# Optimization experiments

Measured on AMD Instinct MI355X. Metric: run time of the kernel, lower is better.

Reference implementation:

```python
import math
import jax, jax.numpy as jnp
import numpy as np

K = 1.0            # Lorentz manifold curvature k
B, S = 4, 2048     # batch, seq_len
IN, H, OUT = 512, 8, 64   # in_channels, num_heads, out_channels (space dim; head_dim = OUT+1)


def setup_inputs() -> dict:
    key = jax.random.key(0)
    ks = jax.random.split(key, 8)
    std = 1.0 / math.sqrt(IN)
    return {
        "query_input": jax.random.normal(ks[0], (B, S, IN), jnp.float32),
        "source_input": jax.random.normal(ks[1], (B, S, IN), jnp.float32),
        # per-head HypLinear weights stacked on a leading head axis: [H, OUT, IN]
        "Wq_w": jax.random.normal(ks[2], (H, OUT, IN), jnp.float32) * std,
        "Wq_b": jnp.zeros((H, OUT), jnp.float32),
        "Wk_w": jax.random.normal(ks[3], (H, OUT, IN), jnp.float32) * std,
        "Wk_b": jnp.zeros((H, OUT), jnp.float32),
        "Wv_w": jax.random.normal(ks[4], (H, OUT, IN), jnp.float32) * std,
        "Wv_b": jnp.zeros((H, OUT), jnp.float32),
        "scale": jnp.array([math.sqrt(OUT)], jnp.float32),  # nn.Parameter([sqrt(out_channels)])
        "bias": jnp.zeros((), jnp.float32),                 # nn.Parameter(zeros(()))
    }


def hyp_linear(x, w, b):
    # HypLinear: linear map to space part, recompute Lorentz time coord sqrt(||x_s||^2 + k)
    sp = jnp.einsum('bsi,hoi->bsho', x, w) + b            # [B,S,H,OUT]
    t = jnp.sqrt(jnp.sum(sp * sp, axis=-1, keepdims=True) + K)
    return jnp.concatenate([t, sp], axis=-1)              # [B,S,H,OUT+1]


def reference(query_input, source_input, Wq_w, Wq_b, Wk_w, Wk_b, Wv_w, Wv_b, scale, bias):
    q = hyp_linear(query_input, Wq_w, Wq_b)   # [B,S,H,D], D = OUT+1
    k = hyp_linear(source_input, Wk_w, Wk_b)
    v = hyp_linear(source_input, Wv_w, Wv_b)

    # Lorentzian cinner: <x,y>_L = -x0*y0 + <x_s, y_s>
    sgn = jnp.concatenate([-jnp.ones((1,), q.dtype), jnp.ones((OUT,), q.dtype)])
    att = jnp.einsum('bqhd,bkhd->bhqk', q * sgn, k)       # [B,H,S,S]
    att = (2.0 + 2.0 * att) / scale[0] + bias

    causal = jnp.triu(jnp.full((S, S), -1e9, q.dtype), 1)  # causal mask (additive)
    att = jax.nn.softmax(att + causal, axis=-1)

    ctx = jnp.einsum('bhqk,bkhd->bqhd', att, v)           # [B,S,H,D]

    # manifold.mid_point over the heads axis (dim=-2)
    ave = jnp.mean(ctx, axis=2)                           # [B,S,D]
    inner = -ave[..., :1] ** 2 + jnp.sum(ave[..., 1:] ** 2, axis=-1, keepdims=True)
    denom = jnp.sqrt(jnp.maximum(jnp.abs(-inner), 1e-8))
    return math.sqrt(K) * ave / denom                     # [B,S,D]
```

## Files before the change

### kernel.cpp

```cpp
#include <hip/hip_runtime.h>

#define BATCH 4
#define SEQ   2048
#define INC   512
#define NH    8
#define OUTC  64
#define DD    65
#define NROW  (BATCH * NH * SEQ)

typedef float f32x4 __attribute__((ext_vector_type(4)));
typedef short short8 __attribute__((ext_vector_type(8)));
typedef short short4v __attribute__((ext_vector_type(4)));
typedef unsigned short us;

static __device__ __forceinline__ us f2b(float f) {
  unsigned int u = __float_as_uint(f);
  u = (u + 0x7FFFu + ((u >> 16) & 1u)) >> 16;
  return (us)u;
}
static __device__ __forceinline__ float b2f(us h) {
  return __uint_as_float(((unsigned int)h) << 16);
}
static __device__ __forceinline__ unsigned int pk2(float lo, float hi) {
  unsigned int r;
  asm("v_cvt_pk_bf16_f32 %0, %1, %2" : "=v"(r) : "v"(lo), "v"(hi));
  return r;
}
static __device__ __forceinline__ short8 mk8(unsigned int a, unsigned int b,
                                             unsigned int c, unsigned int d) {
  union { unsigned int u[4]; short8 s; } x;
  x.u[0] = a; x.u[1] = b; x.u[2] = c; x.u[3] = d;
  return x.s;
}

#define GLDS(g, l) __builtin_amdgcn_global_load_lds( \
    (const __attribute__((address_space(1))) void*)(g), \
    (__attribute__((address_space(3))) void*)(l), 16, 0, 0)
#define SB() __builtin_amdgcn_sched_barrier(0)

__global__ __launch_bounds__(256) void tobf16_kernel(
    const float* __restrict__ Xq, const float* __restrict__ Xs,
    const float* __restrict__ Wq, const float* __restrict__ Wk,
    const float* __restrict__ Wv,
    us* __restrict__ dXq, us* __restrict__ dXs,
    us* __restrict__ dWq, us* __restrict__ dWk, us* __restrict__ dWv)
{
  const int which = blockIdx.y;
  const float* src;
  us* dst;
  int n;
  switch (which) {
    case 0: src = Xq; dst = dXq; n = BATCH * SEQ * INC; break;
    case 1: src = Xs; dst = dXs; n = BATCH * SEQ * INC; break;
    case 2: src = Wq; dst = dWq; n = NH * OUTC * INC; break;
    case 3: src = Wk; dst = dWk; n = NH * OUTC * INC; break;
    default: src = Wv; dst = dWv; n = NH * OUTC * INC; break;
  }
  for (long i = (long)blockIdx.x * 256 + threadIdx.x; i * 4 < n;
       i += (long)gridDim.x * 256) {
    f32x4 v = *(const f32x4*)(src + i * 4);
    short4v o;
    o[0] = (short)f2b(v[0]); o[1] = (short)f2b(v[1]);
    o[2] = (short)f2b(v[2]); o[3] = (short)f2b(v[3]);
    *(short4v*)(dst + i * 4) = o;
  }
}

__global__ __launch_bounds__(256) void proj_kernel(
    const us* __restrict__ Xqb, const us* __restrict__ Xsb,
    const us* __restrict__ Wqb, const us* __restrict__ Wkb, const us* __restrict__ Wvb,
    const float* __restrict__ Bq, const float* __restrict__ Bk, const float* __restrict__ Bv,
    const float* __restrict__ scale_p,
    us* __restrict__ qs, unsigned int* __restrict__ qta,
    us* __restrict__ ks, unsigned int* __restrict__ kta,
    us* __restrict__ vs, us* __restrict__ vtc)
{
  const int which = blockIdx.z;
  const us* X = (which == 0) ? Xqb : Xsb;
  const us* W = (which == 0) ? Wqb : (which == 1 ? Wkb : Wvb);
  const float* Bb = (which == 0) ? Bq : (which == 1 ? Bk : Bv);
  us* outs = (which == 0) ? qs : (which == 1 ? ks : vs);
  const float al2 = (2.0f / scale_p[0]) * 1.44269504088896f;
  const float oscale = (which == 0) ? al2 : 1.0f;

  const int lin = blockIdx.x;
  const int h   = (lin >> 3) & 7;
  const int m0  = (((lin >> 6) << 3) | (lin & 7)) * 64;
  const int n0  = h * 64;

  __shared__ alignas(16) us lX[2][64 * 64];
  __shared__ alignas(16) us lW[2][64 * 64];

  const int tid  = threadIdx.x;
  const int lane = tid & 63;
  const int wave = tid >> 6;
  const int arow = lane & 15;
  const int agrp = lane >> 4;
  const int rl   = lane >> 3;
  const int chx  = ((lane & 7) ^ rl) * 8;
  const int r0   = wave * 8 + rl;
  const int r1   = r0 + 32;

#define PSTAGE(buf, k0) do { \
    GLDS(X + (size_t)(m0 + r0) * INC + (k0) + chx, &lX[buf][wave * 512]); \
    GLDS(X + (size_t)(m0 + r1) * INC + (k0) + chx, &lX[buf][2048 + wave * 512]); \
    GLDS(W + (size_t)(n0 + r0) * INC + (k0) + chx, &lW[buf][wave * 512]); \
    GLDS(W + (size_t)(n0 + r1) * INC + (k0) + chx, &lW[buf][2048 + wave * 512]); \
  } while (0)

  f32x4 acc[4] = {};
  PSTAGE(0, 0);

  for (int kk = 0; kk < 8; ++kk) {
    const int cur = kk & 1;
    if (kk < 7) {
      PSTAGE(cur ^ 1, (kk + 1) * 64);
      asm volatile("s_waitcnt vmcnt(4)");
    } else {
      asm volatile("s_waitcnt vmcnt(0)");
    }
    __builtin_amdgcn_s_barrier();
#pragma unroll
    for (int kc = 0; kc < 2; ++kc) {
      short8 af = *(const short8*)&lX[cur][(wave * 16 + arow) * 64 + (((kc * 4 + agrp) ^ (arow & 7)) * 8)];
#pragma unroll
      for (int c = 0; c < 4; ++c) {
        short8 bf = *(const short8*)&lW[cur][(c * 16 + arow) * 64 + (((kc * 4 + agrp) ^ (arow & 7)) * 8)];
        acc[c] = __builtin_amdgcn_mfma_f32_16x16x32_bf16(af, bf, acc[c], 0, 0, 0);
      }
    }
    __builtin_amdgcn_s_barrier();
  }

  float bcol[4];
#pragma unroll
  for (int c = 0; c < 4; ++c) bcol[c] = Bb[n0 + c * 16 + arow];
#pragma unroll
  for (int r = 0; r < 4; ++r) {
    float s2 = 0.f;
#pragma unroll
    for (int c = 0; c < 4; ++c) {
      float v = acc[c][r] + bcol[c];
      acc[c][r] = v;
      s2 += v * v;
    }
    s2 += __shfl_xor(s2, 1); s2 += __shfl_xor(s2, 2);
    s2 += __shfl_xor(s2, 4); s2 += __shfl_xor(s2, 8);
    float tv = sqrtf(s2 + 1.0f);
    int gs = m0 + wave * 16 + agrp * 4 + r;
    int bi = gs >> 11, si = gs & (SEQ - 1);
    size_t rowbase = (size_t)(bi * NH + h) * SEQ + si;
    size_t obase = rowbase * 64;
#pragma unroll
    for (int c = 0; c < 4; ++c) outs[obase + c * 16 + arow] = f2b(oscale * acc[c][r]);
    if (arow == 0) {
      if (which == 0) {
        float st = al2 * tv;
        us qh = f2b(st);
        us ql = f2b(st - b2f(qh));
        qta[rowbase] = (unsigned int)qh | ((unsigned int)ql << 16);
      } else {
        us th = f2b(tv);
        us tl = f2b(tv - b2f(th));
        if (which == 1) {
          kta[rowbase] = (unsigned int)(us)(th ^ 0x8000)
                       | ((unsigned int)(us)(tl ^ 0x8000) << 16);
        } else {
          vtc[rowbase] = th;
          vtc[NROW + rowbase] = tl;
        }
      }
    }
  }
}

__global__ __launch_bounds__(256) void transpose_v_kernel(
    const us* __restrict__ vs, us* __restrict__ vT)
{
  const int bh = blockIdx.y;
  const int s0 = blockIdx.x * 64;
  __shared__ us lT[64 * 80];
  const int tid = threadIdx.x;
#pragma unroll
  for (int u0 = 0; u0 < 2; ++u0) {
    int u = tid + u0 * 256;
    int row = u >> 3, ch = u & 7;
    short8 v = *(const short8*)&vs[((size_t)bh * SEQ + s0 + row) * 64 + ch * 8];
    *(short8*)&lT[row * 80 + ch * 8] = v;
  }
  __syncthreads();
#pragma unroll
  for (int u0 = 0; u0 < 2; ++u0) {
    int u = tid + u0 * 256;
    int o = u >> 3, sc = u & 7;
    short4v w0, w1;
#pragma unroll
    for (int j = 0; j < 4; ++j) w0[j] = (short)lT[(sc * 8 + j) * 80 + o];
#pragma unroll
    for (int j = 0; j < 4; ++j) w1[j] = (short)lT[(sc * 8 + 4 + j) * 80 + o];
    const int base0 = (sc & 1) * 32 + (sc >> 2) * 8 + ((sc >> 1) & 1) * 4;
    us* dst = vT + ((size_t)bh * 64 + o) * SEQ + s0;
    *(short4v*)(dst + base0) = w0;
    *(short4v*)(dst + base0 + 16) = w1;
  }
}

__global__ __launch_bounds__(256) void attn_kernel(
    const us* __restrict__ qs, const unsigned int* __restrict__ qta,
    const us* __restrict__ ks, const unsigned int* __restrict__ kta,
    const us* __restrict__ vT, const us* __restrict__ vtc,
    float* __restrict__ part)
{
  const int f = blockIdx.x;
  const int xcd = f & 7, idx = f >> 3;
  const int bh = xcd * 4 + (idx >> 5);
  const int inner = idx & 31;
  const int xb = inner >> 1;
  const int hf = inner & 1;

  __shared__ alignas(16) us lK[2][64 * 64];
  __shared__ alignas(16) us lV[2][64 * 64];

  const int tid  = threadIdx.x;
  const int lane = tid & 63;
  const int wave = tid >> 6;
  const int arow = lane & 15;
  const int agrp = lane >> 4;

  const size_t bhbase = (size_t)bh * SEQ;
  const us* kgp = ks + bhbase * 64;
  const us* vgp = vT + (size_t)bh * 64 * SEQ;
  const unsigned int* ktp = kta + bhbase;
  const us* vtp = vtc + (size_t)(arow & 1) * NROW + bhbase;

  const int rl    = lane >> 3;
  const int chx   = ((lane & 7) ^ rl) * 8;
  const int r0s   = wave * 8 + rl;
  const int r1s   = r0s + 32;
  const int dsl0  = (agrp ^ (arow & 7)) * 8;
  const int dsl1  = ((4 + agrp) ^ (arow & 7)) * 8;
  const int dslV0 = ((agrp * 2) ^ (arow & 7)) * 8;
  const int dslV1 = ((agrp * 2 + 1) ^ (arow & 7)) * 8;

#define ASTAGE(buf, t64) do { \
    const int kk = (t64) * 64; \
    GLDS(kgp + (size_t)(kk + r0s) * 64 + chx, &lK[buf][wave * 512]); \
    GLDS(kgp + (size_t)(kk + r1s) * 64 + chx, &lK[buf][2048 + wave * 512]); \
    GLDS(vgp + (size_t)r0s * SEQ + kk + chx, &lV[buf][wave * 512]); \
    GLDS(vgp + (size_t)r1s * SEQ + kk + chx, &lV[buf][2048 + wave * 512]); \
  } while (0)

  short8 ones8, zero8 = {};
#pragma unroll
  for (int j = 0; j < 8; ++j) ones8[j] = (short)0x3F80;

  for (int seg = 0; seg < 2; ++seg) {
    const int qb = seg ? (31 - xb) : xb;
    const int q0 = qb * 64;
    const int c0 = (qb + 2) >> 1;
    const int t_lo = hf ? c0 : 0;
    const int t_hi = hf ? (qb + 1) : c0;
    const int nt = t_hi - t_lo;
    const int wq = wave * 16 + arow;

    f32x4 acc[5] = {};

    if (nt > 0) {
      const us* qp = qs + (bhbase + q0 + wq) * 64;
      short8 qf0 = *(const short8*)(qp + agrp * 8);
      short8 qf1 = *(const short8*)(qp + 32 + agrp * 8);
      unsigned int qw = qta[bhbase + q0 + wq];
      short8 qf2 = {};
      if (agrp == 0) {
        qf2[0] = (short)(qw & 0xFFFFu);
        qf2[1] = (short)(qw & 0xFFFFu);
        qf2[2] = (short)(qw >> 16);
      }

      unsigned int ka[4];
      short4v vaA[2], vaB[2];
      {
        const int kk = t_lo * 64;
#pragma unroll
        for (int c = 0; c < 4; ++c) ka[c] = ktp[kk + c * 16 + arow];
#pragma unroll
        for (int kc = 0; kc < 2; ++kc) {
          vaA[kc] = *(const short4v*)(vtp + kk + kc * 32 + agrp * 4);
          vaB[kc] = *(const short4v*)(vtp + kk + kc * 32 + 16 + agrp * 4);
        }
      }
      SB();
      ASTAGE(0, t_lo);
      SB();

      for (int it = 0; it < nt; ++it) {
        const int t = t_lo + it;
        const int cur = it & 1;
        if (it < nt - 1) {
          ASTAGE(cur ^ 1, t + 1);
          SB();
          if (it == 0) asm volatile("s_waitcnt vmcnt(4)");
          else         asm volatile("s_waitcnt vmcnt(12)");
        } else {
          SB();
          if (nt > 1) asm volatile("s_waitcnt vmcnt(8)");
          else        asm volatile("s_waitcnt vmcnt(0)");
        }
        SB();
        __builtin_amdgcn_s_barrier();

        const us* Kb = lK[cur];
        const us* Vb = lV[cur];

        f32x4 sS[4] = {};
        __builtin_amdgcn_s_setprio(1);
#pragma unroll
        for (int c = 0; c < 4; ++c) {
          short8 kf = *(const short8*)&Kb[(c * 16 + arow) * 64 + dsl0];
          sS[c] = __builtin_amdgcn_mfma_f32_16x16x32_bf16(kf, qf0, sS[c], 0, 0, 0);
        }
#pragma unroll
        for (int c = 0; c < 4; ++c) {
          short8 kf = *(const short8*)&Kb[(c * 16 + arow) * 64 + dsl1];
          sS[c] = __builtin_amdgcn_mfma_f32_16x16x32_bf16(kf, qf1, sS[c], 0, 0, 0);
        }
#pragma unroll
        for (int c = 0; c < 4; ++c) {
          short8 kf2 = {};
          if (agrp == 0) {
            unsigned int w0 = ka[c];
            kf2[0] = (short)(w0 & 0xFFFFu);
            kf2[1] = (short)(w0 >> 16);
            kf2[2] = (short)(w0 & 0xFFFFu);
          }
          sS[c] = __builtin_amdgcn_mfma_f32_16x16x32_bf16(kf2, qf2, sS[c], 0, 0, 0);
        }
        __builtin_amdgcn_s_setprio(0);

#pragma unroll
        for (int c = 0; c < 4; ++c)
#pragma unroll
          for (int r = 0; r < 4; ++r)
            sS[c][r] = exp2f(sS[c][r]);
        if (t == qb) {
#pragma unroll
          for (int c = 0; c < 4; ++c)
#pragma unroll
            for (int r = 0; r < 4; ++r)
              if (c * 16 + agrp * 4 + r > wq) sS[c][r] = 0.f;
        }

        __builtin_amdgcn_s_setprio(1);
#pragma unroll
        for (int kc = 0; kc < 2; ++kc) {
          short8 pf = mk8(pk2(sS[2*kc][0], sS[2*kc][1]),
                          pk2(sS[2*kc][2], sS[2*kc][3]),
                          pk2(sS[2*kc+1][0], sS[2*kc+1][1]),
                          pk2(sS[2*kc+1][2], sS[2*kc+1][3]));
          const int dsl = kc ? dslV1 : dslV0;
#pragma unroll
          for (int dc = 0; dc < 4; ++dc) {
            short8 vf = *(const short8*)&Vb[(dc * 16 + arow) * 64 + dsl];
            acc[dc] = __builtin_amdgcn_mfma_f32_16x16x32_bf16(pf, vf, acc[dc], 0, 0, 0);
          }
          short8 vf4;
          if (arow < 2) {
            *(short4v*)&vf4 = vaA[kc];
            *(((short4v*)&vf4) + 1) = vaB[kc];
          } else vf4 = (arow == 2) ? ones8 : zero8;
          acc[4] = __builtin_amdgcn_mfma_f32_16x16x32_bf16(pf, vf4, acc[4], 0, 0, 0);
        }
        __builtin_amdgcn_s_setprio(0);

        SB();
        if (it + 1 < nt) {
          const int kk = (t + 1) * 64;
#pragma unroll
          for (int c = 0; c < 4; ++c) ka[c] = ktp[kk + c * 16 + arow];
#pragma unroll
          for (int kc = 0; kc < 2; ++kc) {
            vaA[kc] = *(const short4v*)(vtp + kk + kc * 32 + agrp * 4);
            vaB[kc] = *(const short4v*)(vtp + kk + kc * 32 + 16 + agrp * 4);
          }
        }
        SB();
        __builtin_amdgcn_s_barrier();
      }
    }

    const size_t pb = ((size_t)(bh * 32 + qb) * 2 + hf) * 64;
#pragma unroll
    for (int r = 0; r < 4; ++r) {
      float t0 = __shfl(acc[4][r], (agrp << 4) | 0);
      float t1 = __shfl(acc[4][r], (agrp << 4) | 1);
      float ls = __shfl(acc[4][r], (agrp << 4) | 2);
      size_t rp = (pb + wave * 16 + agrp * 4 + r) * 68;
#pragma unroll
      for (int dc = 0; dc < 4; ++dc)
        part[rp + dc * 16 + arow] = acc[dc][r];
      if (arow == 0) {
        part[rp + 64] = t0 + t1;
        part[rp + 65] = ls;
      }
    }
  }
}

__global__ __launch_bounds__(256) void finalize_kernel(
    const float* __restrict__ part, float* __restrict__ out)
{
  const int tid  = threadIdx.x;
  const int lane = tid & 63;
  const int gw = blockIdx.x * 4 + (tid >> 6);
  const int b = gw >> 11, si = gw & (SEQ - 1);
  const int qb = si >> 6, row = si & 63;

  float vsum = 0.f, tsum = 0.f;
#pragma unroll
  for (int h = 0; h < NH; ++h) {
    float Ah = 0.f, Th = 0.f, Lh = 0.f;
#pragma unroll
    for (int hf = 0; hf < 2; ++hf) {
      size_t rb = (((size_t)((b * NH + h) * 32 + qb) * 2 + hf) * 64 + row) * 68;
      Ah += part[rb + lane];
      Th += part[rb + 64];
      Lh += part[rb + 65];
    }
    float inv = 1.0f / Lh;
    vsum = fmaf(Ah, inv, vsum);
    tsum = fmaf(Th, inv, tsum);
  }
  float ave  = vsum * 0.125f;
  float tave = tsum * 0.125f;
  float contrib = ave * ave;
  if (lane == 0) contrib -= tave * tave;
  contrib += __shfl_xor(contrib, 1);
  contrib += __shfl_xor(contrib, 2);
  contrib += __shfl_xor(contrib, 4);
  contrib += __shfl_xor(contrib, 8);
  contrib += __shfl_xor(contrib, 16);
  contrib += __shfl_xor(contrib, 32);
  float denom = sqrtf(fmaxf(fabsf(contrib), 1e-8f));
  size_t ob = ((size_t)b * SEQ + si) * (size_t)DD;
  out[ob + 1 + lane] = ave / denom;
  if (lane == 0) out[ob] = tave / denom;
}

extern "C" void kernel_launch(void* const* d_in, const int* in_sizes, int n_in,
                              void* d_out, int out_size, void* d_ws, size_t ws_size,
                              hipStream_t stream) {
  const float* Xq  = (const float*)d_in[0];
  const float* Xs  = (const float*)d_in[1];
  const float* Wq  = (const float*)d_in[2];
  const float* Bq  = (const float*)d_in[3];
  const float* Wk  = (const float*)d_in[4];
  const float* Bk  = (const float*)d_in[5];
  const float* Wv  = (const float*)d_in[6];
  const float* Bv  = (const float*)d_in[7];
  const float* scale = (const float*)d_in[8];
  float* out = (float*)d_out;

  char* p = (char*)d_ws;

  float* part = (float*)p;
  us* Xqb   = (us*)p;
  us* Xsb   = (us*)(p + 16777216);
  us* Wqb16 = (us*)(p + 33554432);
  us* Wkb16 = (us*)(p + 34078720);
  us* Wvb16 = (us*)(p + 34603008);
  p += (size_t)1024 * 2 * 64 * 68 * 4;
  us* qsb = (us*)p; p += (size_t)NROW * 64 * 2;
  us* ksb = (us*)p; p += (size_t)NROW * 64 * 2;
  us* vsb = (us*)p; p += (size_t)NROW * 64 * 2;
  us* vTb = (us*)p; p += (size_t)NROW * 64 * 2;
  unsigned int* qtaw = (unsigned int*)p; p += (size_t)NROW * 4;
  unsigned int* ktaw = (unsigned int*)p; p += (size_t)NROW * 4;
  us* vtcw = (us*)p; p += (size_t)NROW * 2 * 2;

  tobf16_kernel<<<dim3(1024, 5), 256, 0, stream>>>(
      Xq, Xs, Wq, Wk, Wv, Xqb, Xsb, Wqb16, Wkb16, Wvb16);
  proj_kernel<<<dim3(1024, 1, 3), 256, 0, stream>>>(
      Xqb, Xsb, Wqb16, Wkb16, Wvb16, Bq, Bk, Bv, scale,
      qsb, qtaw, ksb, ktaw, vsb, vtcw);
  transpose_v_kernel<<<dim3(SEQ / 64, BATCH * NH), 256, 0, stream>>>(vsb, vTb);
  attn_kernel<<<dim3(1024), 256, 0, stream>>>(
      qsb, qtaw, ksb, ktaw, vTb, vtcw, part);
  finalize_kernel<<<(BATCH * SEQ) / 4, 256, 0, stream>>>(part, out);
}
```

Baseline: 100.3 us.

## Split attention waves into 2x2 query/key quadrants with LDS P staging

Each wave now handles 32 query rows against half of the 64-key tile instead of 16 query rows against all 64 keys. Each K fragment read from LDS feeds two MFMAs, one per query set. The P matrix is staged through per-wave LDS so its layout matches the new V fragment reads. The V transpose kernel now writes plain contiguous rows instead of the interleaved order. Partial outputs from the two key-halves are reduced through LDS before writing, which adds extra barriers and LDS traffic and is meant to halve K fragment LDS reads per query.

```diff
diff --git a/kernel.cpp b/kernel.cpp
--- a/kernel.cpp
+++ b/kernel.cpp
@@ -25,12 +25,6 @@
   unsigned int r;
   asm("v_cvt_pk_bf16_f32 %0, %1, %2" : "=v"(r) : "v"(lo), "v"(hi));
   return r;
-}
-static __device__ __forceinline__ short8 mk8(unsigned int a, unsigned int b,
-                                             unsigned int c, unsigned int d) {
-  union { unsigned int u[4]; short8 s; } x;
-  x.u[0] = a; x.u[1] = b; x.u[2] = c; x.u[3] = d;
-  return x.s;
 }
 
 #define GLDS(g, l) __builtin_amdgcn_global_load_lds( \
@@ -193,15 +187,10 @@
   for (int u0 = 0; u0 < 2; ++u0) {
     int u = tid + u0 * 256;
     int o = u >> 3, sc = u & 7;
-    short4v w0, w1;
-#pragma unroll
-    for (int j = 0; j < 4; ++j) w0[j] = (short)lT[(sc * 8 + j) * 80 + o];
-#pragma unroll
-    for (int j = 0; j < 4; ++j) w1[j] = (short)lT[(sc * 8 + 4 + j) * 80 + o];
-    const int base0 = (sc & 1) * 32 + (sc >> 2) * 8 + ((sc >> 1) & 1) * 4;
-    us* dst = vT + ((size_t)bh * 64 + o) * SEQ + s0;
-    *(short4v*)(dst + base0) = w0;
-    *(short4v*)(dst + base0 + 16) = w1;
+    short8 w;
+#pragma unroll
+    for (int j = 0; j < 8; ++j) w[j] = lT[(sc * 8 + j) * 80 + o];
+    *(short8*)&vT[((size_t)bh * 64 + o) * SEQ + s0 + sc * 8] = w;
   }
 }
 
@@ -220,12 +209,15 @@
 
   __shared__ alignas(16) us lK[2][64 * 64];
   __shared__ alignas(16) us lV[2][64 * 64];
+  __shared__ alignas(16) us lP[4][32 * 40];
 
   const int tid  = threadIdx.x;
   const int lane = tid & 63;
   const int wave = tid >> 6;
   const int arow = lane & 15;
   const int agrp = lane >> 4;
+  const int qh   = wave >> 1;
+  const int kh   = wave & 1;
 
   const size_t bhbase = (size_t)bh * SEQ;
   const us* kgp = ks + bhbase * 64;
@@ -233,14 +225,16 @@
   const unsigned int* ktp = kta + bhbase;
   const us* vtp = vtc + (size_t)(arow & 1) * NROW + bhbase;
 
-  const int rl    = lane >> 3;
-  const int chx   = ((lane & 7) ^ rl) * 8;
-  const int r0s   = wave * 8 + rl;
-  const int r1s   = r0s + 32;
-  const int dsl0  = (agrp ^ (arow & 7)) * 8;
-  const int dsl1  = ((4 + agrp) ^ (arow & 7)) * 8;
-  const int dslV0 = ((agrp * 2) ^ (arow & 7)) * 8;
-  const int dslV1 = ((agrp * 2 + 1) ^ (arow & 7)) * 8;
+  const int rl   = lane >> 3;
+  const int chx  = ((lane & 7) ^ rl) * 8;
+  const int r0s  = wave * 8 + rl;
+  const int r1s  = r0s + 32;
+  const int dsl0 = (agrp ^ (arow & 7)) * 8;
+  const int dsl1 = ((4 + agrp) ^ (arow & 7)) * 8;
+  const int dslK = (((kh << 2) + agrp) ^ (arow & 7)) * 8;
+  us* myP = &lP[wave][0];
+  const int pw0 = arow * 40 + agrp * 4;
+  const int prd = arow * 40 + agrp * 8;
 
 #define ASTAGE(buf, t64) do { \
     const int kk = (t64) * 64; \
@@ -261,33 +255,36 @@
     const int t_lo = hf ? c0 : 0;
     const int t_hi = hf ? (qb + 1) : c0;
     const int nt = t_hi - t_lo;
-    const int wq = wave * 16 + arow;
-
-    f32x4 acc[5] = {};
+
+    f32x4 acc[2][4] = {};
+    f32x4 ac4[2] = {};
 
     if (nt > 0) {
-      const us* qp = qs + (bhbase + q0 + wq) * 64;
-      short8 qf0 = *(const short8*)(qp + agrp * 8);
-      short8 qf1 = *(const short8*)(qp + 32 + agrp * 8);
-      unsigned int qw = qta[bhbase + q0 + wq];
-      short8 qf2 = {};
+      int wq0 = q0 + qh * 32 + arow;
+      int wq1 = wq0 + 16;
+      const us* qp0 = qs + (bhbase + wq0) * 64;
+      const us* qp1 = qs + (bhbase + wq1) * 64;
+      short8 qf0a = *(const short8*)(qp0 + agrp * 8);
+      short8 qf1a = *(const short8*)(qp0 + 32 + agrp * 8);
+      short8 qf0b = *(const short8*)(qp1 + agrp * 8);
+      short8 qf1b = *(const short8*)(qp1 + 32 + agrp * 8);
+      unsigned int qwa = qta[bhbase + wq0];
+      unsigned int qwb = qta[bhbase + wq1];
+      short8 qf2a = {}, qf2b = {};
       if (agrp == 0) {
-        qf2[0] = (short)(qw & 0xFFFFu);
-        qf2[1] = (short)(qw & 0xFFFFu);
-        qf2[2] = (short)(qw >> 16);
-      }
-
-      unsigned int ka[4];
-      short4v vaA[2], vaB[2];
+        qf2a[0] = (short)(qwa & 0xFFFFu); qf2a[1] = (short)(qwa & 0xFFFFu);
+        qf2a[2] = (short)(qwa >> 16);
+        qf2b[0] = (short)(qwb & 0xFFFFu); qf2b[1] = (short)(qwb & 0xFFFFu);
+        qf2b[2] = (short)(qwb >> 16);
+      }
+
+      unsigned int ka0, ka1;
+      short8 va;
       {
-        const int kk = t_lo * 64;
-#pragma unroll
-        for (int c = 0; c < 4; ++c) ka[c] = ktp[kk + c * 16 + arow];
-#pragma unroll
-        for (int kc = 0; kc < 2; ++kc) {
-          vaA[kc] = *(const short4v*)(vtp + kk + kc * 32 + agrp * 4);
-          vaB[kc] = *(const short4v*)(vtp + kk + kc * 32 + 16 + agrp * 4);
-        }
+        const int kk = t_lo * 64 + kh * 32;
+        ka0 = ktp[kk + arow];
+        ka1 = ktp[kk + 16 + arow];
+        va = *(const short8*)(vtp + kk + agrp * 8);
       }
       SB();
       ASTAGE(0, t_lo);
@@ -300,10 +297,10 @@
           ASTAGE(cur ^ 1, t + 1);
           SB();
           if (it == 0) asm volatile("s_waitcnt vmcnt(4)");
-          else         asm volatile("s_waitcnt vmcnt(12)");
+          else         asm volatile("s_waitcnt vmcnt(7)");
         } else {
           SB();
-          if (nt > 1) asm volatile("s_waitcnt vmcnt(8)");
+          if (nt > 1) asm volatile("s_waitcnt vmcnt(3)");
           else        asm volatile("s_waitcnt vmcnt(0)");
         }
         SB();
@@ -312,96 +309,133 @@
         const us* Kb = lK[cur];
         const us* Vb = lV[cur];
 
-        f32x4 sS[4] = {};
+        f32x4 sa[2] = {}, sb[2] = {};
         __builtin_amdgcn_s_setprio(1);
 #pragma unroll
-        for (int c = 0; c < 4; ++c) {
-          short8 kf = *(const short8*)&Kb[(c * 16 + arow) * 64 + dsl0];
-          sS[c] = __builtin_amdgcn_mfma_f32_16x16x32_bf16(kf, qf0, sS[c], 0, 0, 0);
-        }
-#pragma unroll
-        for (int c = 0; c < 4; ++c) {
-          short8 kf = *(const short8*)&Kb[(c * 16 + arow) * 64 + dsl1];
-          sS[c] = __builtin_amdgcn_mfma_f32_16x16x32_bf16(kf, qf1, sS[c], 0, 0, 0);
-        }
-#pragma unroll
-        for (int c = 0; c < 4; ++c) {
+        for (int c = 0; c < 2; ++c) {
+          short8 kf = *(const short8*)&Kb[(kh * 32 + c * 16 + arow) * 64 + dsl0];
+          sa[c] = __builtin_amdgcn_mfma_f32_16x16x32_bf16(kf, qf0a, sa[c], 0, 0, 0);
+          sb[c] = __builtin_amdgcn_mfma_f32_16x16x32_bf16(kf, qf0b, sb[c], 0, 0, 0);
+        }
+#pragma unroll
+        for (int c = 0; c < 2; ++c) {
+          short8 kf = *(const short8*)&Kb[(kh * 32 + c * 16 + arow) * 64 + dsl1];
+          sa[c] = __builtin_amdgcn_mfma_f32_16x16x32_bf16(kf, qf1a, sa[c], 0, 0, 0);
+          sb[c] = __builtin_amdgcn_mfma_f32_16x16x32_bf16(kf, qf1b, sb[c], 0, 0, 0);
+        }
+#pragma unroll
+        for (int c = 0; c < 2; ++c) {
           short8 kf2 = {};
           if (agrp == 0) {
-            unsigned int w0 = ka[c];
+            unsigned int w0 = c ? ka1 : ka0;
             kf2[0] = (short)(w0 & 0xFFFFu);
             kf2[1] = (short)(w0 >> 16);
             kf2[2] = (short)(w0 & 0xFFFFu);
           }
-          sS[c] = __builtin_amdgcn_mfma_f32_16x16x32_bf16(kf2, qf2, sS[c], 0, 0, 0);
+          sa[c] = __builtin_amdgcn_mfma_f32_16x16x32_bf16(kf2, qf2a, sa[c], 0, 0, 0);
+          sb[c] = __builtin_amdgcn_mfma_f32_16x16x32_bf16(kf2, qf2b, sb[c], 0, 0, 0);
         }
         __builtin_amdgcn_s_setprio(0);
 
 #pragma unroll
-        for (int c = 0; c < 4; ++c)
-#pragma unroll
-          for (int r = 0; r < 4; ++r)
-            sS[c][r] = exp2f(sS[c][r]);
+        for (int c = 0; c < 2; ++c)
+#pragma unroll
+          for (int r = 0; r < 4; ++r) {
+            sa[c][r] = exp2f(sa[c][r]);
+            sb[c][r] = exp2f(sb[c][r]);
+          }
         if (t == qb) {
-#pragma unroll
-          for (int c = 0; c < 4; ++c)
-#pragma unroll
-            for (int r = 0; r < 4; ++r)
-              if (c * 16 + agrp * 4 + r > wq) sS[c][r] = 0.f;
-        }
-
+          const int kb = t * 64 + kh * 32;
+#pragma unroll
+          for (int c = 0; c < 2; ++c)
+#pragma unroll
+            for (int r = 0; r < 4; ++r) {
+              int k = kb + c * 16 + agrp * 4 + r;
+              if (k > q0 + qh * 32 + arow)      sa[c][r] = 0.f;
+              if (k > q0 + qh * 32 + 16 + arow) sb[c][r] = 0.f;
+            }
+        }
+
+        {
+          typedef unsigned int uint2v __attribute__((ext_vector_type(2)));
+          uint2v w;
+          w[0] = pk2(sa[0][0], sa[0][1]); w[1] = pk2(sa[0][2], sa[0][3]);
+          *(uint2v*)&myP[pw0] = w;
+          w[0] = pk2(sa[1][0], sa[1][1]); w[1] = pk2(sa[1][2], sa[1][3]);
+          *(uint2v*)&myP[pw0 + 16] = w;
+          w[0] = pk2(sb[0][0], sb[0][1]); w[1] = pk2(sb[0][2], sb[0][3]);
+          *(uint2v*)&myP[640 + pw0] = w;
+          w[0] = pk2(sb[1][0], sb[1][1]); w[1] = pk2(sb[1][2], sb[1][3]);
+          *(uint2v*)&myP[640 + pw0 + 16] = w;
+        }
         __builtin_amdgcn_s_setprio(1);
-#pragma unroll
-        for (int kc = 0; kc < 2; ++kc) {
-          short8 pf = mk8(pk2(sS[2*kc][0], sS[2*kc][1]),
-                          pk2(sS[2*kc][2], sS[2*kc][3]),
-                          pk2(sS[2*kc+1][0], sS[2*kc+1][1]),
-                          pk2(sS[2*kc+1][2], sS[2*kc+1][3]));
-          const int dsl = kc ? dslV1 : dslV0;
+        {
+          short8 pfa = *(const short8*)&myP[prd];
+          short8 pfb = *(const short8*)&myP[640 + prd];
 #pragma unroll
           for (int dc = 0; dc < 4; ++dc) {
-            short8 vf = *(const short8*)&Vb[(dc * 16 + arow) * 64 + dsl];
-            acc[dc] = __builtin_amdgcn_mfma_f32_16x16x32_bf16(pf, vf, acc[dc], 0, 0, 0);
+            short8 vf = *(const short8*)&Vb[(dc * 16 + arow) * 64 + dslK];
+            acc[0][dc] = __builtin_amdgcn_mfma_f32_16x16x32_bf16(pfa, vf, acc[0][dc], 0, 0, 0);
+            acc[1][dc] = __builtin_amdgcn_mfma_f32_16x16x32_bf16(pfb, vf, acc[1][dc], 0, 0, 0);
           }
-          short8 vf4;
-          if (arow < 2) {
-            *(short4v*)&vf4 = vaA[kc];
-            *(((short4v*)&vf4) + 1) = vaB[kc];
-          } else vf4 = (arow == 2) ? ones8 : zero8;
-          acc[4] = __builtin_amdgcn_mfma_f32_16x16x32_bf16(pf, vf4, acc[4], 0, 0, 0);
+          short8 vf4 = (arow < 2) ? va : ((arow == 2) ? ones8 : zero8);
+          ac4[0] = __builtin_amdgcn_mfma_f32_16x16x32_bf16(pfa, vf4, ac4[0], 0, 0, 0);
+          ac4[1] = __builtin_amdgcn_mfma_f32_16x16x32_bf16(pfb, vf4, ac4[1], 0, 0, 0);
         }
         __builtin_amdgcn_s_setprio(0);
 
         SB();
         if (it + 1 < nt) {
-          const int kk = (t + 1) * 64;
-#pragma unroll
-          for (int c = 0; c < 4; ++c) ka[c] = ktp[kk + c * 16 + arow];
-#pragma unroll
-          for (int kc = 0; kc < 2; ++kc) {
-            vaA[kc] = *(const short4v*)(vtp + kk + kc * 32 + agrp * 4);
-            vaB[kc] = *(const short4v*)(vtp + kk + kc * 32 + 16 + agrp * 4);
-          }
+          const int kk = (t + 1) * 64 + kh * 32;
+          ka0 = ktp[kk + arow];
+          ka1 = ktp[kk + 16 + arow];
+          va = *(const short8*)(vtp + kk + agrp * 8);
         }
         SB();
         __builtin_amdgcn_s_barrier();
       }
     }
 
-    const size_t pb = ((size_t)(bh * 32 + qb) * 2 + hf) * 64;
-#pragma unroll
-    for (int r = 0; r < 4; ++r) {
-      float t0 = __shfl(acc[4][r], (agrp << 4) | 0);
-      float t1 = __shfl(acc[4][r], (agrp << 4) | 1);
-      float ls = __shfl(acc[4][r], (agrp << 4) | 2);
-      size_t rp = (pb + wave * 16 + agrp * 4 + r) * 68;
-#pragma unroll
-      for (int dc = 0; dc < 4; ++dc)
-        part[rp + dc * 16 + arow] = acc[dc][r];
-      if (arow == 0) {
-        part[rp + 64] = t0 + t1;
-        part[rp + 65] = ls;
-      }
+    __syncthreads();
+    {
+      float* mq = (float*)&lK[0][0] + (size_t)qh * 2048;
+      float* ma = (float*)&lP[0][0] + (size_t)qh * 128;
+      if (kh == 0) {
+#pragma unroll
+        for (int qset = 0; qset < 2; ++qset)
+#pragma unroll
+          for (int r = 0; r < 4; ++r) {
+            int ql = qset * 16 + agrp * 4 + r;
+#pragma unroll
+            for (int dc = 0; dc < 4; ++dc)
+              mq[ql * 64 + dc * 16 + arow] = acc[qset][dc][r];
+            if (arow < 3) ma[ql * 4 + arow] = ac4[qset][r];
+          }
+      }
+      __syncthreads();
+      if (kh == 1) {
+        const size_t pb = ((size_t)(bh * 32 + qb) * 2 + hf) * 64;
+#pragma unroll
+        for (int qset = 0; qset < 2; ++qset)
+#pragma unroll
+          for (int r = 0; r < 4; ++r) {
+            int ql = qset * 16 + agrp * 4 + r;
+            float av = ac4[qset][r] + ((arow < 3) ? ma[ql * 4 + arow] : 0.f);
+            float t0 = __shfl(av, (agrp << 4) | 0);
+            float t1 = __shfl(av, (agrp << 4) | 1);
+            float ls = __shfl(av, (agrp << 4) | 2);
+            size_t rp = (pb + qh * 32 + ql) * 68;
+#pragma unroll
+            for (int dc = 0; dc < 4; ++dc)
+              part[rp + dc * 16 + arow] =
+                  acc[qset][dc][r] + mq[ql * 64 + dc * 16 + arow];
+            if (arow == 0) {
+              part[rp + 64] = t0 + t1;
+              part[rp + 65] = ls;
+            }
+          }
+      }
+      __syncthreads();
     }
   }
 }
```

Result: slower. 104.7 us (+4.4%).

## Use 128-row query tiles with 8 waves and three-way balanced KV split

Applied to the files above, without the earlier changes.

The attention kernel now runs 512-thread blocks covering 128 query rows, so each staged K/V tile is reused by twice as many rows. Causal work is spread over three balanced KV-range segments per paired query tile, with the partial buffers and finalize reduction reshaped to match. The P matrix is routed through a per-wave LDS scratch tile instead of register packing, the V transpose drops its permuted layout, and vsb is aliased into the workspace. In exchange there are fewer blocks (768) and higher per-block LDS and register use, which may cut occupancy, plus extra LDS round trips for P.

```diff
diff --git a/kernel.cpp b/kernel.cpp
--- a/kernel.cpp
+++ b/kernel.cpp
@@ -11,6 +11,7 @@
 typedef float f32x4 __attribute__((ext_vector_type(4)));
 typedef short short8 __attribute__((ext_vector_type(8)));
 typedef short short4v __attribute__((ext_vector_type(4)));
+typedef unsigned int uint2v __attribute__((ext_vector_type(2)));
 typedef unsigned short us;
 
 static __device__ __forceinline__ us f2b(float f) {
@@ -25,12 +26,6 @@
   unsigned int r;
   asm("v_cvt_pk_bf16_f32 %0, %1, %2" : "=v"(r) : "v"(lo), "v"(hi));
   return r;
-}
-static __device__ __forceinline__ short8 mk8(unsigned int a, unsigned int b,
-                                             unsigned int c, unsigned int d) {
-  union { unsigned int u[4]; short8 s; } x;
-  x.u[0] = a; x.u[1] = b; x.u[2] = c; x.u[3] = d;
-  return x.s;
 }
 
 #define GLDS(g, l) __builtin_amdgcn_global_load_lds( \
@@ -193,19 +188,14 @@
   for (int u0 = 0; u0 < 2; ++u0) {
     int u = tid + u0 * 256;
     int o = u >> 3, sc = u & 7;
-    short4v w0, w1;
-#pragma unroll
-    for (int j = 0; j < 4; ++j) w0[j] = (short)lT[(sc * 8 + j) * 80 + o];
-#pragma unroll
-    for (int j = 0; j < 4; ++j) w1[j] = (short)lT[(sc * 8 + 4 + j) * 80 + o];
-    const int base0 = (sc & 1) * 32 + (sc >> 2) * 8 + ((sc >> 1) & 1) * 4;
-    us* dst = vT + ((size_t)bh * 64 + o) * SEQ + s0;
-    *(short4v*)(dst + base0) = w0;
-    *(short4v*)(dst + base0 + 16) = w1;
-  }
-}
-
-__global__ __launch_bounds__(256) void attn_kernel(
+    short8 w;
+#pragma unroll
+    for (int j = 0; j < 8; ++j) w[j] = lT[(sc * 8 + j) * 80 + o];
+    *(short8*)&vT[((size_t)bh * 64 + o) * SEQ + s0 + sc * 8] = w;
+  }
+}
+
+__global__ __launch_bounds__(512) void attn_kernel(
     const us* __restrict__ qs, const unsigned int* __restrict__ qta,
     const us* __restrict__ ks, const unsigned int* __restrict__ kta,
     const us* __restrict__ vT, const us* __restrict__ vtc,
@@ -213,13 +203,16 @@
 {
   const int f = blockIdx.x;
   const int xcd = f & 7, idx = f >> 3;
-  const int bh = xcd * 4 + (idx >> 5);
-  const int inner = idx & 31;
-  const int xb = inner >> 1;
-  const int hf = inner & 1;
+  const int bh = xcd * 4 + (idx / 24);
+  const int inner = idx % 24;
+  const int x = inner / 3;
+  const int s = inner % 3;
+  const int n0 = 2 * x + 2;
+  const int n1 = 32 - 2 * x;
 
   __shared__ alignas(16) us lK[2][64 * 64];
   __shared__ alignas(16) us lV[2][64 * 64];
+  __shared__ alignas(16) us lP[8][16 * 40];
 
   const int tid  = threadIdx.x;
   const int lane = tid & 63;
@@ -233,21 +226,18 @@
   const unsigned int* ktp = kta + bhbase;
   const us* vtp = vtc + (size_t)(arow & 1) * NROW + bhbase;
 
-  const int rl    = lane >> 3;
-  const int chx   = ((lane & 7) ^ rl) * 8;
-  const int r0s   = wave * 8 + rl;
-  const int r1s   = r0s + 32;
-  const int dsl0  = (agrp ^ (arow & 7)) * 8;
-  const int dsl1  = ((4 + agrp) ^ (arow & 7)) * 8;
-  const int dslV0 = ((agrp * 2) ^ (arow & 7)) * 8;
-  const int dslV1 = ((agrp * 2 + 1) ^ (arow & 7)) * 8;
+  const int rl   = lane >> 3;
+  const int chx  = ((lane & 7) ^ rl) * 8;
+  const int dsl0 = (agrp ^ (arow & 7)) * 8;
+  const int dsl1 = ((4 + agrp) ^ (arow & 7)) * 8;
+  us* myP = &lP[wave][0];
+  const int pw0 = arow * 40 + agrp * 4;
+  const int prd = arow * 40 + agrp * 8;
 
 #define ASTAGE(buf, t64) do { \
     const int kk = (t64) * 64; \
-    GLDS(kgp + (size_t)(kk + r0s) * 64 + chx, &lK[buf][wave * 512]); \
-    GLDS(kgp + (size_t)(kk + r1s) * 64 + chx, &lK[buf][2048 + wave * 512]); \
-    GLDS(vgp + (size_t)r0s * SEQ + kk + chx, &lV[buf][wave * 512]); \
-    GLDS(vgp + (size_t)r1s * SEQ + kk + chx, &lV[buf][2048 + wave * 512]); \
+    GLDS(kgp + (size_t)(kk + wave * 8 + rl) * 64 + chx, &lK[buf][wave * 512]); \
+    GLDS(vgp + (size_t)(wave * 8 + rl) * SEQ + kk + chx, &lV[buf][wave * 512]); \
   } while (0)
 
   short8 ones8, zero8 = {};
@@ -255,140 +245,144 @@
   for (int j = 0; j < 8; ++j) ones8[j] = (short)0x3F80;
 
   for (int seg = 0; seg < 2; ++seg) {
-    const int qb = seg ? (31 - xb) : xb;
-    const int q0 = qb * 64;
-    const int c0 = (qb + 2) >> 1;
-    const int t_lo = hf ? c0 : 0;
-    const int t_hi = hf ? (qb + 1) : c0;
-    const int nt = t_hi - t_lo;
-    const int wq = wave * 16 + arow;
-
+    const int qT = seg ? (15 - x) : x;
+    int lo, hi;
+    if (seg == 0) { lo = min(12 * s, n0);          hi = min(12 * s + 12, n0); }
+    else          { lo = max(12 * s - n0, 0);      hi = min(12 * s + 12 - n0, n1); }
+    const int nt = hi - lo;
+    if (nt <= 0) continue;
+
+    const int wq = qT * 128 + wave * 16 + arow;
     f32x4 acc[5] = {};
 
-    if (nt > 0) {
-      const us* qp = qs + (bhbase + q0 + wq) * 64;
-      short8 qf0 = *(const short8*)(qp + agrp * 8);
-      short8 qf1 = *(const short8*)(qp + 32 + agrp * 8);
-      unsigned int qw = qta[bhbase + q0 + wq];
-      short8 qf2 = {};
-      if (agrp == 0) {
-        qf2[0] = (short)(qw & 0xFFFFu);
-        qf2[1] = (short)(qw & 0xFFFFu);
-        qf2[2] = (short)(qw >> 16);
-      }
-
-      unsigned int ka[4];
-      short4v vaA[2], vaB[2];
+    const us* qp = qs + (bhbase + wq) * 64;
+    short8 qf0 = *(const short8*)(qp + agrp * 8);
+    short8 qf1 = *(const short8*)(qp + 32 + agrp * 8);
+    unsigned int qw = qta[bhbase + wq];
+    short8 qf2 = {};
+    if (agrp == 0) {
+      qf2[0] = (short)(qw & 0xFFFFu);
+      qf2[1] = (short)(qw & 0xFFFFu);
+      qf2[2] = (short)(qw >> 16);
+    }
+
+    unsigned int ka[4];
+    short8 va0, va1;
+    {
+      const int kk = lo * 64;
+#pragma unroll
+      for (int c = 0; c < 4; ++c) ka[c] = ktp[kk + c * 16 + arow];
+      va0 = *(const short8*)(vtp + kk + agrp * 8);
+      va1 = *(const short8*)(vtp + kk + 32 + agrp * 8);
+    }
+    SB();
+    ASTAGE(0, lo);
+    SB();
+
+    for (int it = 0; it < nt; ++it) {
+      const int t = lo + it;
+      const int cur = it & 1;
+      if (it < nt - 1) {
+        ASTAGE(cur ^ 1, t + 1);
+        SB();
+        asm volatile("s_waitcnt vmcnt(2)");
+      } else {
+        SB();
+        asm volatile("s_waitcnt vmcnt(0)");
+      }
+      SB();
+      __builtin_amdgcn_s_barrier();
+
+      const us* Kb = lK[cur];
+      const us* Vb = lV[cur];
+
+      f32x4 sS[4] = {};
+      __builtin_amdgcn_s_setprio(1);
+#pragma unroll
+      for (int c = 0; c < 4; ++c) {
+        short8 kf = *(const short8*)&Kb[(c * 16 + arow) * 64 + dsl0];
+        sS[c] = __builtin_amdgcn_mfma_f32_16x16x32_bf16(kf, qf0, sS[c], 0, 0, 0);
+      }
+#pragma unroll
+      for (int c = 0; c < 4; ++c) {
+        short8 kf = *(const short8*)&Kb[(c * 16 + arow) * 64 + dsl1];
+        sS[c] = __builtin_amdgcn_mfma_f32_16x16x32_bf16(kf, qf1, sS[c], 0, 0, 0);
+      }
+#pragma unroll
+      for (int c = 0; c < 4; ++c) {
+        short8 kf2 = {};
+        if (agrp == 0) {
+          unsigned int w0 = ka[c];
+          kf2[0] = (short)(w0 & 0xFFFFu);
+          kf2[1] = (short)(w0 >> 16);
+          kf2[2] = (short)(w0 & 0xFFFFu);
+        }
+        sS[c] = __builtin_amdgcn_mfma_f32_16x16x32_bf16(kf2, qf2, sS[c], 0, 0, 0);
+      }
+      __builtin_amdgcn_s_setprio(0);
+
+#pragma unroll
+      for (int c = 0; c < 4; ++c)
+#pragma unroll
+        for (int r = 0; r < 4; ++r)
+          sS[c][r] = exp2f(sS[c][r]);
+      if (t >= 2 * qT) {
+        const int kb = t * 64;
+#pragma unroll
+        for (int c = 0; c < 4; ++c)
+#pragma unroll
+          for (int r = 0; r < 4; ++r)
+            if (kb + c * 16 + agrp * 4 + r > wq) sS[c][r] = 0.f;
+      }
+
       {
-        const int kk = t_lo * 64;
+        uint2v w;
+        w[0] = pk2(sS[0][0], sS[0][1]); w[1] = pk2(sS[0][2], sS[0][3]);
+        *(uint2v*)&myP[pw0] = w;
+        w[0] = pk2(sS[1][0], sS[1][1]); w[1] = pk2(sS[1][2], sS[1][3]);
+        *(uint2v*)&myP[pw0 + 16] = w;
+        short8 pf = *(const short8*)&myP[prd];
+        __builtin_amdgcn_s_setprio(1);
+#pragma unroll
+        for (int dc = 0; dc < 4; ++dc) {
+          short8 vf = *(const short8*)&Vb[(dc * 16 + arow) * 64 + dsl0];
+          acc[dc] = __builtin_amdgcn_mfma_f32_16x16x32_bf16(pf, vf, acc[dc], 0, 0, 0);
+        }
+        short8 vf4 = (arow < 2) ? va0 : ((arow == 2) ? ones8 : zero8);
+        acc[4] = __builtin_amdgcn_mfma_f32_16x16x32_bf16(pf, vf4, acc[4], 0, 0, 0);
+        __builtin_amdgcn_s_setprio(0);
+      }
+      {
+        uint2v w;
+        w[0] = pk2(sS[2][0], sS[2][1]); w[1] = pk2(sS[2][2], sS[2][3]);
+        *(uint2v*)&myP[pw0] = w;
+        w[0] = pk2(sS[3][0], sS[3][1]); w[1] = pk2(sS[3][2], sS[3][3]);
+        *(uint2v*)&myP[pw0 + 16] = w;
+        short8 pf = *(const short8*)&myP[prd];
+        __builtin_amdgcn_s_setprio(1);
+#pragma unroll
+        for (int dc = 0; dc < 4; ++dc) {
+          short8 vf = *(const short8*)&Vb[(dc * 16 + arow) * 64 + dsl1];
+          acc[dc] = __builtin_amdgcn_mfma_f32_16x16x32_bf16(pf, vf, acc[dc], 0, 0, 0);
+        }
+        short8 vf4 = (arow < 2) ? va1 : ((arow == 2) ? ones8 : zero8);
+        acc[4] = __builtin_amdgcn_mfma_f32_16x16x32_bf16(pf, vf4, acc[4], 0, 0, 0);
+        __builtin_amdgcn_s_setprio(0);
+      }
+
+      SB();
+      if (it + 1 < nt) {
+        const int kk = (t + 1) * 64;
 #pragma unroll
         for (int c = 0; c < 4; ++c) ka[c] = ktp[kk + c * 16 + arow];
-#pragma unroll
-        for (int kc = 0; kc < 2; ++kc) {
-          vaA[kc] = *(const short4v*)(vtp + kk + kc * 32 + agrp * 4);
-          vaB[kc] = *(const short4v*)(vtp + kk + kc * 32 + 16 + agrp * 4);
-        }
+        va0 = *(const short8*)(vtp + kk + agrp * 8);
+        va1 = *(const short8*)(vtp + kk + 32 + agrp * 8);
       }
       SB();
-      ASTAGE(0, t_lo);
-      SB();
-
-      for (int it = 0; it < nt; ++it) {
-        const int t = t_lo + it;
-        const int cur = it & 1;
-        if (it < nt - 1) {
-          ASTAGE(cur ^ 1, t + 1);
-          SB();
-          if (it == 0) asm volatile("s_waitcnt vmcnt(4)");
-          else         asm volatile("s_waitcnt vmcnt(12)");
-        } else {
-          SB();
-          if (nt > 1) asm volatile("s_waitcnt vmcnt(8)");
-          else        asm volatile("s_waitcnt vmcnt(0)");
-        }
-        SB();
-        __builtin_amdgcn_s_barrier();
-
-        const us* Kb = lK[cur];
-        const us* Vb = lV[cur];
-
-        f32x4 sS[4] = {};
-        __builtin_amdgcn_s_setprio(1);
-#pragma unroll
-        for (int c = 0; c < 4; ++c) {
-          short8 kf = *(const short8*)&Kb[(c * 16 + arow) * 64 + dsl0];
-          sS[c] = __builtin_amdgcn_mfma_f32_16x16x32_bf16(kf, qf0, sS[c], 0, 0, 0);
-        }
-#pragma unroll
-        for (int c = 0; c < 4; ++c) {
-          short8 kf = *(const short8*)&Kb[(c * 16 + arow) * 64 + dsl1];
-          sS[c] = __builtin_amdgcn_mfma_f32_16x16x32_bf16(kf, qf1, sS[c], 0, 0, 0);
-        }
-#pragma unroll
-        for (int c = 0; c < 4; ++c) {
-          short8 kf2 = {};
-          if (agrp == 0) {
-            unsigned int w0 = ka[c];
-            kf2[0] = (short)(w0 & 0xFFFFu);
-            kf2[1] = (short)(w0 >> 16);
-            kf2[2] = (short)(w0 & 0xFFFFu);
-          }
-          sS[c] = __builtin_amdgcn_mfma_f32_16x16x32_bf16(kf2, qf2, sS[c], 0, 0, 0);
-        }
-        __builtin_amdgcn_s_setprio(0);
-
-#pragma unroll
-        for (int c = 0; c < 4; ++c)
-#pragma unroll
-          for (int r = 0; r < 4; ++r)
-            sS[c][r] = exp2f(sS[c][r]);
-        if (t == qb) {
-#pragma unroll
-          for (int c = 0; c < 4; ++c)
-#pragma unroll
-            for (int r = 0; r < 4; ++r)
-              if (c * 16 + agrp * 4 + r > wq) sS[c][r] = 0.f;
-        }
-
-        __builtin_amdgcn_s_setprio(1);
-#pragma unroll
-        for (int kc = 0; kc < 2; ++kc) {
-          short8 pf = mk8(pk2(sS[2*kc][0], sS[2*kc][1]),
-                          pk2(sS[2*kc][2], sS[2*kc][3]),
-                          pk2(sS[2*kc+1][0], sS[2*kc+1][1]),
-                          pk2(sS[2*kc+1][2], sS[2*kc+1][3]));
-          const int dsl = kc ? dslV1 : dslV0;
-#pragma unroll
-          for (int dc = 0; dc < 4; ++dc) {
-            short8 vf = *(const short8*)&Vb[(dc * 16 + arow) * 64 + dsl];
-            acc[dc] = __builtin_amdgcn_mfma_f32_16x16x32_bf16(pf, vf, acc[dc], 0, 0, 0);
-          }
-          short8 vf4;
-          if (arow < 2) {
-            *(short4v*)&vf4 = vaA[kc];
-            *(((short4v*)&vf4) + 1) = vaB[kc];
-          } else vf4 = (arow == 2) ? ones8 : zero8;
-          acc[4] = __builtin_amdgcn_mfma_f32_16x16x32_bf16(pf, vf4, acc[4], 0, 0, 0);
-        }
-        __builtin_amdgcn_s_setprio(0);
-
-        SB();
-        if (it + 1 < nt) {
-          const int kk = (t + 1) * 64;
-#pragma unroll
-          for (int c = 0; c < 4; ++c) ka[c] = ktp[kk + c * 16 + arow];
-#pragma unroll
-          for (int kc = 0; kc < 2; ++kc) {
-            vaA[kc] = *(const short4v*)(vtp + kk + kc * 32 + agrp * 4);
-            vaB[kc] = *(const short4v*)(vtp + kk + kc * 32 + 16 + agrp * 4);
-          }
-        }
-        SB();
-        __builtin_amdgcn_s_barrier();
-      }
-    }
-
-    const size_t pb = ((size_t)(bh * 32 + qb) * 2 + hf) * 64;
+      __builtin_amdgcn_s_barrier();
+    }
+
+    const size_t pb = ((size_t)(bh * 16 + qT) * 3 + s) * 128;
 #pragma unroll
     for (int r = 0; r < 4; ++r) {
       float t0 = __shfl(acc[4][r], (agrp << 4) | 0);
@@ -413,18 +407,28 @@
   const int lane = tid & 63;
   const int gw = blockIdx.x * 4 + (tid >> 6);
   const int b = gw >> 11, si = gw & (SEQ - 1);
-  const int qb = si >> 6, row = si & 63;
+  const int qT = si >> 7, row = si & 127;
+
+  const bool v0 = (qT <= 7) || (qT >= 11);
+  const bool v1 = (qT >= 6);
+  const bool v2 = (qT >= 8);
 
   float vsum = 0.f, tsum = 0.f;
 #pragma unroll
   for (int h = 0; h < NH; ++h) {
+    const size_t tb = ((size_t)(b * NH + h) * 16 + qT) * 3;
     float Ah = 0.f, Th = 0.f, Lh = 0.f;
-#pragma unroll
-    for (int hf = 0; hf < 2; ++hf) {
-      size_t rb = (((size_t)((b * NH + h) * 32 + qb) * 2 + hf) * 64 + row) * 68;
-      Ah += part[rb + lane];
-      Th += part[rb + 64];
-      Lh += part[rb + 65];
+    if (v0) {
+      size_t rb = ((tb + 0) * 128 + row) * 68;
+      Ah += part[rb + lane]; Th += part[rb + 64]; Lh += part[rb + 65];
+    }
+    if (v1) {
+      size_t rb = ((tb + 1) * 128 + row) * 68;
+      Ah += part[rb + lane]; Th += part[rb + 64]; Lh += part[rb + 65];
+    }
+    if (v2) {
+      size_t rb = ((tb + 2) * 128 + row) * 68;
+      Ah += part[rb + lane]; Th += part[rb + 64]; Lh += part[rb + 65];
     }
     float inv = 1.0f / Lh;
     vsum = fmaf(Ah, inv, vsum);
@@ -468,10 +472,10 @@
   us* Wqb16 = (us*)(p + 33554432);
   us* Wkb16 = (us*)(p + 34078720);
   us* Wvb16 = (us*)(p + 34603008);
-  p += (size_t)1024 * 2 * 64 * 68 * 4;
+  us* vsb   = (us*)(p + 35651584);
+  p += (size_t)32 * 16 * 3 * 128 * 68 * 4;
   us* qsb = (us*)p; p += (size_t)NROW * 64 * 2;
   us* ksb = (us*)p; p += (size_t)NROW * 64 * 2;
-  us* vsb = (us*)p; p += (size_t)NROW * 64 * 2;
   us* vTb = (us*)p; p += (size_t)NROW * 64 * 2;
   unsigned int* qtaw = (unsigned int*)p; p += (size_t)NROW * 4;
   unsigned int* ktaw = (unsigned int*)p; p += (size_t)NROW * 4;
@@ -483,7 +487,7 @@
       Xqb, Xsb, Wqb16, Wkb16, Wvb16, Bq, Bk, Bv, scale,
       qsb, qtaw, ksb, ktaw, vsb, vtcw);
   transpose_v_kernel<<<dim3(SEQ / 64, BATCH * NH), 256, 0, stream>>>(vsb, vTb);
-  attn_kernel<<<dim3(1024), 256, 0, stream>>>(
+  attn_kernel<<<dim3(768), 512, 0, stream>>>(
       qsb, qtaw, ksb, ktaw, vTb, vtcw, part);
   finalize_kernel<<<(BATCH * SEQ) / 4, 256, 0, stream>>>(part, out);
 }
```

Result: no change. 100.4 us (+0.1%).
